# Kernel optimization log

Hardware: AMD Instinct MI355X
Metric: run time of the kernel (lower is better)

## Reference

```python
import jax, jax.numpy as jnp
import numpy as np

CH = 128
DQK = CH // 8  # 16


def setup_inputs() -> dict:
    key = jax.random.key(0)
    ks = jax.random.split(key, 8)
    B, H, W, C = 4, 64, 64, CH
    inputs = jax.random.normal(ks[0], (B, H, W, C), dtype=jnp.float32)
    # 1x1 conv weights == dense over channel dim
    wq = jax.random.normal(ks[1], (C, DQK), dtype=jnp.float32) * (1.0 / np.sqrt(C))
    bq = jnp.zeros((DQK,), dtype=jnp.float32)
    wk = jax.random.normal(ks[2], (C, DQK), dtype=jnp.float32) * (1.0 / np.sqrt(C))
    bk = jnp.zeros((DQK,), dtype=jnp.float32)
    wv = jax.random.normal(ks[3], (C, C), dtype=jnp.float32) * (1.0 / np.sqrt(C))
    bv = jnp.zeros((C,), dtype=jnp.float32)
    gamma = jnp.zeros((1,), dtype=jnp.float32)
    return {"inputs": inputs, "wq": wq, "bq": bq, "wk": wk, "bk": bk,
            "wv": wv, "bv": bv, "gamma": gamma}


def reference(inputs, wq, bq, wk, bk, wv, bv, gamma):
    B, H, W, C = inputs.shape
    N = H * W
    x = inputs.reshape(B, N, C)  # flatten spatial
    q = x @ wq + bq              # [B, N, d]
    k = x @ wk + bk              # [B, N, d]
    v = x @ wv + bv              # [B, N, C]
    # full N x N attention (no scaling, per SAGAN source)
    scores = jnp.einsum('bnd,bmd->bnm', q, k)
    attn = jax.nn.softmax(scores, axis=-1)
    out = jnp.einsum('bnm,bmc->bnc', attn, v).reshape(B, H, W, C)
    return gamma * out + inputs
```

## Files before the change

### kernel.cpp

```cpp
#include <hip/hip_runtime.h>
#include <hip/hip_bf16.h>


typedef __attribute__((ext_vector_type(4)))  short short4v;
typedef __attribute__((ext_vector_type(8)))  short short8;
typedef __attribute__((ext_vector_type(16))) float f32x16;
typedef unsigned short u16;

#define LOG2E 1.4426950408889634f

#define GLOAD_LDS16(g, l)                                                     \
  __builtin_amdgcn_global_load_lds(                                           \
      (const __attribute__((address_space(1))) void*)(g),                     \
      (__attribute__((address_space(3))) void*)(l), 16, 0, 0)

__device__ __forceinline__ u16 f2bf(float f) {
  __hip_bfloat16 h = __float2bfloat16(f);
  return __builtin_bit_cast(u16, h);
}
__device__ __forceinline__ u16 f2bf_fast(float f) {
  unsigned u = __builtin_bit_cast(unsigned, f) + 0x8000u;
  return (u16)(u >> 16);
}
__device__ __forceinline__ float bf2f(u16 u) {
  unsigned v = (unsigned)u << 16;
  return __builtin_bit_cast(float, v);
}
__device__ __forceinline__ float fexp2(float x) {
#if __has_builtin(__builtin_amdgcn_exp2f)
  return __builtin_amdgcn_exp2f(x);
#else
  return exp2f(x);
#endif
}
__device__ __forceinline__ unsigned pkbf(float lo, float hi) {
  unsigned a = __builtin_bit_cast(unsigned, lo) + 0x8000u;
  unsigned b = __builtin_bit_cast(unsigned, hi) + 0x8000u;
  unsigned r;
  asm("v_perm_b32 %0, %1, %2, %3" : "=v"(r) : "v"(b), "v"(a), "s"(0x07060302u));
  return r;
}
__device__ __forceinline__ float xhalf_sum(float x) {
  float a = x, b = x;
  asm("v_permlane32_swap_b32 %0, %1" : "+v"(a), "+v"(b));
  return a + b;
}

__global__ __launch_bounds__(256) void qkv_proj(
    const float* __restrict__ x,
    const float* __restrict__ wq, const float* __restrict__ bq,
    const float* __restrict__ wk, const float* __restrict__ bk,
    const float* __restrict__ wv, const float* __restrict__ bv,
    u16* __restrict__ Qb, u16* __restrict__ Kb, u16* __restrict__ Vt)
{
  __shared__ u16 xs[128 * 136];
  __shared__ u16 ws[160 * 136];
  const int tid  = threadIdx.x;
  const int b    = blockIdx.x >> 6;
  const int n0   = ((blockIdx.x >> 1) & 31) * 128;
  const int half = blockIdx.x & 1;

  const float4* xg = (const float4*)(x + ((size_t)b * 4096 + n0) * 128);
#pragma unroll
  for (int p = 0; p < 16; ++p) {
    int idx = tid + p * 256;
    float4 v = xg[idx];
    int n = idx >> 5, i4 = idx & 31;
    short4v pk;
    pk[0] = (short)f2bf(v.x); pk[1] = (short)f2bf(v.y);
    pk[2] = (short)f2bf(v.z); pk[3] = (short)f2bf(v.w);
    *(short4v*)(xs + n * 136 + i4 * 4) = pk;
  }
  if (half == 0) {
#pragma unroll
    for (int p = 0; p < 8; ++p) {
      int idx = tid + p * 256;
      int k = idx >> 4, d = idx & 15;
      ws[d * 136 + k]        = f2bf(wq[idx] * LOG2E);
      ws[(16 + d) * 136 + k] = f2bf(wk[idx]);
    }
#pragma unroll
    for (int p = 0; p < 32; ++p) {
      int idx = tid + p * 256;
      int k = idx >> 6, c = idx & 63;
      ws[(32 + c) * 136 + k] = f2bf(wv[k * 128 + c]);
    }
  } else {
#pragma unroll
    for (int p = 0; p < 32; ++p) {
      int idx = tid + p * 256;
      int k = idx >> 6, c = 64 + (idx & 63);
      ws[(32 + c) * 136 + k] = f2bf(wv[k * 128 + c]);
    }
  }
  __syncthreads();

  const int lane = tid & 63, wid = tid >> 6;
  const int ln31 = lane & 31, hi = lane >> 5;
  const int NJ = half ? 2 : 3;

#pragma unroll 1
  for (int j = 0; j < NJ; ++j) {
    int t = wid + j * 4;
    int mt, nt;
    if (half == 0) { mt = t / 3; nt = t % 3; }
    else           { mt = t >> 1; nt = 3 + (t & 1); }
    const u16* arow = xs + (mt * 32 + ln31) * 136 + hi * 8;
    const u16* brow = ws + (nt * 32 + ln31) * 136 + hi * 8;
    f32x16 acc = (f32x16)0.0f;
#pragma unroll
    for (int ks = 0; ks < 8; ++ks) {
      short8 a = *(const short8*)(arow + ks * 16);
      short8 w = *(const short8*)(brow + ks * 16);
      acc = __builtin_amdgcn_mfma_f32_32x32x16_bf16(a, w, acc, 0, 0, 0);
    }
    if (nt == 0) {
      float bias = (ln31 < 16) ? bq[ln31] * LOG2E : bk[ln31 & 15];
      u16* base = ((ln31 < 16) ? Qb : Kb)
                + ((size_t)b * 4096 + n0 + mt * 32) * 16 + (ln31 & 15);
#pragma unroll
      for (int r = 0; r < 16; ++r) {
        int nl = (r & 3) + 8 * (r >> 2) + 4 * hi;
        base[nl * 16] = f2bf(acc[r] + bias);
      }
    } else {
      int c = (nt - 1) * 32 + ln31;
      float bias = bv[c];
      u16* vb = Vt + ((size_t)b * 128 + c) * 4096 + n0 + mt * 32 + 4 * hi;
#pragma unroll
      for (int g = 0; g < 4; ++g) {
        short4v pk;
        pk[0] = (short)f2bf(acc[g*4+0] + bias);
        pk[1] = (short)f2bf(acc[g*4+1] + bias);
        pk[2] = (short)f2bf(acc[g*4+2] + bias);
        pk[3] = (short)f2bf(acc[g*4+3] + bias);
        *(short4v*)(vb + 8 * g) = pk;
      }
    }
  }
}

template<int NKS>
__global__ __launch_bounds__(256, 3) void attn(
    const u16* __restrict__ Qb, const u16* __restrict__ Kb,
    const u16* __restrict__ Vt,
    u16* __restrict__ Ob, float* __restrict__ Lp)
{
  __shared__ __align__(16) char sm[2][16384];
  const int tid  = threadIdx.x;
  const int lane = tid & 63;
  const int wid  = tid >> 6;
  const int ln31 = lane & 31;
  const int hi   = lane >> 5;

  const int bx   = blockIdx.x;
  const int ks   = bx % NKS;
  const int rest = bx / NKS;
  const int b    = rest >> 5;
  const int qt   = rest & 31;
  const int qw   = qt * 128 + wid * 32;
  const int c0   = (ks * 64) / NKS;
  const int c1   = ((ks + 1) * 64) / NKS;

  const short8 qf = *(const short8*)(Qb + (((size_t)b * 4096 + qw + ln31) << 4) + (hi << 3));

  f32x16 acc[4];
#pragma unroll
  for (int ct = 0; ct < 4; ++ct) acc[ct] = (f32x16)0.0f;
  float lacc = 0.f;
  const f32x16 cbias = (f32x16)(-16.0f);

  const char* kg = (const char*)(Kb + (size_t)b * 4096 * 16);
  const char* vsrc = (const char*)(Vt + (size_t)b * 128 * 4096)
                   + (size_t)(wid * 32 + (lane >> 3)) * 8192
                   + (((lane & 7) ^ (lane >> 3)) << 4);

  uint4 rk0, rk1;
  short8 paA0, paA1, paB0, paB1;

  auto stageV = [&](char* buf, int ck) {
    char* ldst = buf + wid * 4096 + (lane << 4);
    const char* g = vsrc + (size_t)ck * 128;
#pragma unroll
    for (int c = 0; c < 4; ++c)
      GLOAD_LDS16(g + c * 65536, ldst + c * 1024);
  };
  auto loadK = [&](int kb) {
    const char* kr = kg + (size_t)(kb + ln31) * 32 + hi * 16;
    rk0 = *(const uint4*)(kr);
    rk1 = *(const uint4*)(kr + 1024);
  };

  auto computeP = [&]() {
#pragma unroll
    for (int kt = 0; kt < 2; ++kt) {
      short8 kf = __builtin_bit_cast(short8, kt ? rk1 : rk0);
      f32x16 s = __builtin_amdgcn_mfma_f32_32x32x16_bf16(kf, qf, cbias, 0, 0, 0);

      float e0 = fexp2(s[0]),  e1 = fexp2(s[1]);
      unsigned u0 = pkbf(e0, e1);  float t0 = e0 + e1;
      float e2 = fexp2(s[2]),  e3 = fexp2(s[3]);
      unsigned u1 = pkbf(e2, e3);  float t1 = e2 + e3;
      float e4 = fexp2(s[4]),  e5 = fexp2(s[5]);
      unsigned u2 = pkbf(e4, e5);  float t2 = e4 + e5;
      float e6 = fexp2(s[6]),  e7 = fexp2(s[7]);
      unsigned u3 = pkbf(e6, e7);  float t3 = e6 + e7;
      float e8 = fexp2(s[8]),  e9 = fexp2(s[9]);
      unsigned y0 = pkbf(e8, e9);  float t4 = e8 + e9;
      float ea = fexp2(s[10]), eb = fexp2(s[11]);
      unsigned y1 = pkbf(ea, eb);  float t5 = ea + eb;
      float ec = fexp2(s[12]), ed = fexp2(s[13]);
      unsigned y2 = pkbf(ec, ed);  float t6 = ec + ed;
      float ee = fexp2(s[14]), ef = fexp2(s[15]);
      unsigned y3 = pkbf(ee, ef);  float t7 = ee + ef;
      lacc += ((t0 + t1) + (t2 + t3)) + ((t4 + t5) + (t6 + t7));

      asm("v_permlane32_swap_b32 %0, %1" : "+v"(u0), "+v"(u2));
      asm("v_permlane32_swap_b32 %0, %1" : "+v"(u1), "+v"(u3));
      asm("v_permlane32_swap_b32 %0, %1" : "+v"(y0), "+v"(y2));
      asm("v_permlane32_swap_b32 %0, %1" : "+v"(y1), "+v"(y3));
      union { unsigned u[4]; short8 s8; } f0, f1;
      f0.u[0] = u0; f0.u[1] = u1; f0.u[2] = u2; f0.u[3] = u3;
      f1.u[0] = y0; f1.u[1] = y1; f1.u[2] = y2; f1.u[3] = y3;
      if (kt == 0) { paA0 = f0.s8; paA1 = f1.s8; }
      else         { paB0 = f0.s8; paB1 = f1.s8; }
    }
  };

  auto doPV = [&](const char* buf) {
    const int sw = ln31 & 7;
    __builtin_amdgcn_s_setprio(1);
#pragma unroll
    for (int ct = 0; ct < 4; ++ct) {
      const char* vrow = buf + ct * 4096 + ln31 * 128;
      short8 v00 = *(const short8*)(vrow + (((hi)     ^ sw) << 4));
      short8 v01 = *(const short8*)(vrow + (((hi + 2) ^ sw) << 4));
      short8 v10 = *(const short8*)(vrow + (((hi + 4) ^ sw) << 4));
      short8 v11 = *(const short8*)(vrow + (((hi + 6) ^ sw) << 4));
      acc[ct] = __builtin_amdgcn_mfma_f32_32x32x16_bf16(paA0, v00, acc[ct], 0, 0, 0);
      acc[ct] = __builtin_amdgcn_mfma_f32_32x32x16_bf16(paA1, v01, acc[ct], 0, 0, 0);
      acc[ct] = __builtin_amdgcn_mfma_f32_32x32x16_bf16(paB0, v10, acc[ct], 0, 0, 0);
      acc[ct] = __builtin_amdgcn_mfma_f32_32x32x16_bf16(paB1, v11, acc[ct], 0, 0, 0);
    }
    __builtin_amdgcn_s_setprio(0);
  };

  stageV(sm[0], c0);
  loadK(c0 * 64);
  __syncthreads();
  computeP();
  int cur = 0;
#pragma unroll 1
  for (int it = c0; it < c1; ++it) {
    if (it < c1 - 1) {
      stageV(sm[cur ^ 1], it + 1);
      loadK((it + 1) * 64);
    }
    doPV(sm[cur]);
    if (it < c1 - 1) {
      __syncthreads();
      computeP();
    }
    cur ^= 1;
  }

  float lt = xhalf_sum(lacc);
  if (lane < 32)
    Lp[(size_t)ks * 16384 + (size_t)b * 4096 + qw + lane] = lt;
  u16* Op = Ob + ((size_t)ks * 16384 + (size_t)b * 4096 + qw) * 128;
#pragma unroll
  for (int ct = 0; ct < 4; ++ct) {
#pragma unroll
    for (int r = 0; r < 16; ++r) {
      int q = (r & 3) + 8 * (r >> 2) + 4 * hi;
      Op[(size_t)q * 128 + ct * 32 + ln31] = f2bf_fast(acc[ct][r]);
    }
  }
}

template<int NKS>
__global__ __launch_bounds__(256) void combine(
    const u16* __restrict__ Ob, const float* __restrict__ Lp,
    const float* __restrict__ x, const float* __restrict__ gamma,
    float* __restrict__ out)
{
  int i    = blockIdx.x * 256 + threadIdx.x;
  int nrow = i >> 4;
  int c0   = (i & 15) << 3;

  float wsum = 0.f;
#pragma unroll
  for (int p = 0; p < NKS; ++p) wsum += Lp[(size_t)p * 16384 + nrow];
  float inv = gamma[0] / wsum;

  size_t off = (size_t)nrow * 128 + c0;
  float accv[8];
#pragma unroll
  for (int j = 0; j < 8; ++j) accv[j] = 0.f;
#pragma unroll
  for (int p = 0; p < NKS; ++p) {
    short8 v = *(const short8*)(Ob + (size_t)p * 16384 * 128 + off);
#pragma unroll
    for (int j = 0; j < 8; ++j) accv[j] += bf2f((u16)v[j]);
  }
  float4 xa = *(const float4*)(x + off);
  float4 xb = *(const float4*)(x + off + 4);
  float4 ra, rb;
  ra.x = fmaf(accv[0], inv, xa.x); ra.y = fmaf(accv[1], inv, xa.y);
  ra.z = fmaf(accv[2], inv, xa.z); ra.w = fmaf(accv[3], inv, xa.w);
  rb.x = fmaf(accv[4], inv, xb.x); rb.y = fmaf(accv[5], inv, xb.y);
  rb.z = fmaf(accv[6], inv, xb.z); rb.w = fmaf(accv[7], inv, xb.w);
  *(float4*)(out + off)     = ra;
  *(float4*)(out + off + 4) = rb;
}

extern "C" void kernel_launch(void* const* d_in, const int* in_sizes, int n_in,
                              void* d_out, int out_size, void* d_ws, size_t ws_size,
                              hipStream_t stream)
{
  const float* x  = (const float*)d_in[0];
  const float* wq = (const float*)d_in[1];
  const float* bq = (const float*)d_in[2];
  const float* wk = (const float*)d_in[3];
  const float* bk = (const float*)d_in[4];
  const float* wv = (const float*)d_in[5];
  const float* bv = (const float*)d_in[6];
  const float* gm = (const float*)d_in[7];

  char* w = (char*)d_ws;
  u16*   Qb = (u16*)(w);
  u16*   Kb = (u16*)(w + (512ll << 10));
  u16*   Vt = (u16*)(w + (1ll << 20));
  u16*   Ob = (u16*)(w + (5ll << 20));
  float* out = (float*)d_out;

  qkv_proj<<<256, 256, 0, stream>>>(x, wq, bq, wk, bk, wv, bv, Qb, Kb, Vt);

  const size_t need8 = (5ll << 20) + 8ll * (4ll << 20) + 8ll * 16384 * 4;
  const size_t need4 = (5ll << 20) + 4ll * (4ll << 20) + 4ll * 16384 * 4;
  if (ws_size >= need8) {
    float* Lp = (float*)(w + (5ll << 20) + 8ll * (4ll << 20));
    attn<8><<<1024, 256, 0, stream>>>(Qb, Kb, Vt, Ob, Lp);
    combine<8><<<1024, 256, 0, stream>>>(Ob, Lp, x, gm, out);
  } else if (ws_size >= need4) {
    float* Lp = (float*)(w + (5ll << 20) + 4ll * (4ll << 20));
    attn<4><<<512, 256, 0, stream>>>(Qb, Kb, Vt, Ob, Lp);
    combine<4><<<1024, 256, 0, stream>>>(Ob, Lp, x, gm, out);
  } else {
    float* Lp = (float*)(w + (5ll << 20) + 2ll * (4ll << 20));
    attn<2><<<256, 256, 0, stream>>>(Qb, Kb, Vt, Ob, Lp);
    combine<2><<<1024, 256, 0, stream>>>(Ob, Lp, x, gm, out);
  }
}
```

Measured before the change: 50.05 us.

## Read V directly from global in single-wave attention blocks with XCD-aware mapping

```diff
diff --git a/kernel.cpp b/kernel.cpp
--- a/kernel.cpp
+++ b/kernel.cpp
@@ -8,11 +8,6 @@
 typedef unsigned short u16;
 
 #define LOG2E 1.4426950408889634f
-
-#define GLOAD_LDS16(g, l)                                                     \
-  __builtin_amdgcn_global_load_lds(                                           \
-      (const __attribute__((address_space(1))) void*)(g),                     \
-      (__attribute__((address_space(3))) void*)(l), 16, 0, 0)
 
 __device__ __forceinline__ u16 f2bf(float f) {
   __hip_bfloat16 h = __float2bfloat16(f);
@@ -141,26 +136,25 @@
 }
 
 template<int NKS>
-__global__ __launch_bounds__(256, 3) void attn(
+__global__ __launch_bounds__(64) void attn(
     const u16* __restrict__ Qb, const u16* __restrict__ Kb,
     const u16* __restrict__ Vt,
     u16* __restrict__ Ob, float* __restrict__ Lp)
 {
-  __shared__ __align__(16) char sm[2][16384];
-  const int tid  = threadIdx.x;
-  const int lane = tid & 63;
-  const int wid  = tid >> 6;
+  const int lane = threadIdx.x;
   const int ln31 = lane & 31;
   const int hi   = lane >> 5;
 
-  const int bx   = blockIdx.x;
-  const int ks   = bx % NKS;
-  const int rest = bx / NKS;
-  const int b    = rest >> 5;
-  const int qt   = rest & 31;
-  const int qw   = qt * 128 + wid * 32;
-  const int c0   = (ks * 64) / NKS;
-  const int c1   = ((ks + 1) * 64) / NKS;
+  constexpr int KH  = NKS / 2;
+  constexpr int KHL = (NKS == 8) ? 2 : 1;
+  const int bid  = blockIdx.x;
+  const int xcd  = bid & 7;
+  const int b    = xcd >> 1;
+  const int rest = bid >> 3;
+  const int qw   = (rest >> KHL) * 32;
+  const int ks   = (xcd & 1) * KH + (rest & (KH - 1));
+  const int c0   = ks * (64 / NKS);
+  const int c1   = (ks + 1) * (64 / NKS);
 
   const short8 qf = *(const short8*)(Qb + (((size_t)b * 4096 + qw + ln31) << 4) + (hi << 3));
 
@@ -170,21 +164,12 @@
   float lacc = 0.f;
   const f32x16 cbias = (f32x16)(-16.0f);
 
+  const char* vg = (const char*)(Vt + (size_t)b * 128 * 4096);
   const char* kg = (const char*)(Kb + (size_t)b * 4096 * 16);
-  const char* vsrc = (const char*)(Vt + (size_t)b * 128 * 4096)
-                   + (size_t)(wid * 32 + (lane >> 3)) * 8192
-                   + (((lane & 7) ^ (lane >> 3)) << 4);
 
   uint4 rk0, rk1;
   short8 paA0, paA1, paB0, paB1;
 
-  auto stageV = [&](char* buf, int ck) {
-    char* ldst = buf + wid * 4096 + (lane << 4);
-    const char* g = vsrc + (size_t)ck * 128;
-#pragma unroll
-    for (int c = 0; c < 4; ++c)
-      GLOAD_LDS16(g + c * 65536, ldst + c * 1024);
-  };
   auto loadK = [&](int kb) {
     const char* kr = kg + (size_t)(kb + ln31) * 32 + hi * 16;
     rk0 = *(const uint4*)(kr);
@@ -227,41 +212,29 @@
     }
   };
 
-  auto doPV = [&](const char* buf) {
-    const int sw = ln31 & 7;
-    __builtin_amdgcn_s_setprio(1);
+  auto doPV = [&](int it) {
 #pragma unroll
     for (int ct = 0; ct < 4; ++ct) {
-      const char* vrow = buf + ct * 4096 + ln31 * 128;
-      short8 v00 = *(const short8*)(vrow + (((hi)     ^ sw) << 4));
-      short8 v01 = *(const short8*)(vrow + (((hi + 2) ^ sw) << 4));
-      short8 v10 = *(const short8*)(vrow + (((hi + 4) ^ sw) << 4));
-      short8 v11 = *(const short8*)(vrow + (((hi + 6) ^ sw) << 4));
+      const char* vrow = vg + (size_t)(ct * 32 + ln31) * 8192
+                       + (size_t)it * 128 + hi * 16;
+      short8 v00 = *(const short8*)(vrow);
+      short8 v01 = *(const short8*)(vrow + 32);
+      short8 v10 = *(const short8*)(vrow + 64);
+      short8 v11 = *(const short8*)(vrow + 96);
       acc[ct] = __builtin_amdgcn_mfma_f32_32x32x16_bf16(paA0, v00, acc[ct], 0, 0, 0);
       acc[ct] = __builtin_amdgcn_mfma_f32_32x32x16_bf16(paA1, v01, acc[ct], 0, 0, 0);
       acc[ct] = __builtin_amdgcn_mfma_f32_32x32x16_bf16(paB0, v10, acc[ct], 0, 0, 0);
       acc[ct] = __builtin_amdgcn_mfma_f32_32x32x16_bf16(paB1, v11, acc[ct], 0, 0, 0);
     }
-    __builtin_amdgcn_s_setprio(0);
   };
 
-  stageV(sm[0], c0);
   loadK(c0 * 64);
-  __syncthreads();
   computeP();
-  int cur = 0;
 #pragma unroll 1
   for (int it = c0; it < c1; ++it) {
-    if (it < c1 - 1) {
-      stageV(sm[cur ^ 1], it + 1);
-      loadK((it + 1) * 64);
-    }
-    doPV(sm[cur]);
-    if (it < c1 - 1) {
-      __syncthreads();
-      computeP();
-    }
-    cur ^= 1;
+    if (it < c1 - 1) loadK((it + 1) * 64);
+    doPV(it);
+    if (it < c1 - 1) computeP();
   }
 
   float lt = xhalf_sum(lacc);
@@ -340,15 +313,15 @@
   const size_t need4 = (5ll << 20) + 4ll * (4ll << 20) + 4ll * 16384 * 4;
   if (ws_size >= need8) {
     float* Lp = (float*)(w + (5ll << 20) + 8ll * (4ll << 20));
-    attn<8><<<1024, 256, 0, stream>>>(Qb, Kb, Vt, Ob, Lp);
+    attn<8><<<4096, 64, 0, stream>>>(Qb, Kb, Vt, Ob, Lp);
     combine<8><<<1024, 256, 0, stream>>>(Ob, Lp, x, gm, out);
   } else if (ws_size >= need4) {
     float* Lp = (float*)(w + (5ll << 20) + 4ll * (4ll << 20));
-    attn<4><<<512, 256, 0, stream>>>(Qb, Kb, Vt, Ob, Lp);
+    attn<4><<<2048, 64, 0, stream>>>(Qb, Kb, Vt, Ob, Lp);
     combine<4><<<1024, 256, 0, stream>>>(Ob, Lp, x, gm, out);
   } else {
     float* Lp = (float*)(w + (5ll << 20) + 2ll * (4ll << 20));
-    attn<2><<<256, 256, 0, stream>>>(Qb, Kb, Vt, Ob, Lp);
+    attn<2><<<1024, 64, 0, stream>>>(Qb, Kb, Vt, Ob, Lp);
     combine<2><<<1024, 256, 0, stream>>>(Ob, Lp, x, gm, out);
   }
 }
```

New measurement: 91.38 us. 82.6% more time.
